# Kernel optimization log

Hardware: AMD Instinct MI355X
Metric: run time of the kernel (lower is better)

## Reference

```python
import jax, jax.numpy as jnp
import numpy as np

N_HEAD = 16

def setup_inputs() -> dict:
    key = jax.random.key(0)
    ks = jax.random.split(key, 5)
    B, S, D = 4, 2048, 1024
    return {
        "string": jax.random.normal(ks[0], (B, S, D), dtype=jnp.float32),
        "string_len": jax.random.randint(ks[1], (B,), 1, S + 1),
        "Wqkv": jax.random.normal(ks[2], (D, 3 * D), dtype=jnp.float32) * 0.02,
        "bqkv": jnp.zeros((3 * D,), dtype=jnp.float32),
        "Wo": jax.random.normal(ks[3], (D, D), dtype=jnp.float32) * 0.02,
        "bo": jnp.zeros((D,), dtype=jnp.float32),
    }


def reference(string, string_len, Wqkv, bqkv, Wo, bo):
    B, S, D = string.shape
    H = N_HEAD
    hd = D // H
    x = string @ Wqkv + bqkv                      # [B,S,3D]
    q, k, v = jnp.split(x, 3, axis=-1)
    # split heads -> [B,H,S,hd]
    q = q.reshape(B, S, H, hd).transpose(0, 2, 1, 3)
    k = k.reshape(B, S, H, hd).transpose(0, 2, 1, 3)
    v = v.reshape(B, S, H, hd).transpose(0, 2, 1, 3)
    w = jnp.einsum('bhqd,bhkd->bhqk', q, k) / jnp.sqrt(jnp.float32(hd))
    causal = jnp.tril(jnp.ones((S, S), dtype=bool))  # [S,S]
    w = jnp.where(causal[None, None], w, jnp.float32(-1e9))
    w = jax.nn.softmax(w, axis=-1)
    a = jnp.einsum('bhqk,bhkd->bhqd', w, v)       # [B,H,S,hd]
    a = a.transpose(0, 2, 1, 3).reshape(B, S, D)  # merge heads
    a = a @ Wo + bo
    return a, string_len
```

## Files before the change

### kernel.cpp

```cpp
#include <hip/hip_runtime.h>
#include <hip/hip_fp8.h>
#include <stdint.h>

typedef __attribute__((ext_vector_type(8))) short bf16x8;
typedef __attribute__((ext_vector_type(4))) float f32x4;
typedef __attribute__((ext_vector_type(16))) float f32x16;
typedef __attribute__((ext_vector_type(4))) unsigned short u16x4;

static constexpr int Bn = 4, Sn = 2048, Dn = 1024, Hn = 16, HD = 64;
static constexpr int Mrows = Bn * Sn;
static constexpr int D3 = 3 * Dn;

__device__ __forceinline__ unsigned short f2bf(float f) {
  unsigned int u = __float_as_uint(f);
  u += 0x7FFF + ((u >> 16) & 1);
  return (unsigned short)(u >> 16);
}

__device__ __forceinline__ unsigned char f2fp8(float f) {
  __hip_fp8_e4m3 v(f);
  return (unsigned char)v.__x;
}

__device__ __forceinline__ void gload16(const void* gptr, void* lptr) {
  __builtin_amdgcn_global_load_lds(
      (__attribute__((address_space(1))) void*)gptr,
      (__attribute__((address_space(3))) void*)lptr, 16, 0, 0);
}

__device__ __forceinline__ int swz8(int r) { return (r ^ (r >> 3)) & 7; }

__device__ __forceinline__ float vexp2(float x) {
#if __has_builtin(__builtin_amdgcn_exp2f)
  return __builtin_amdgcn_exp2f(x);
#else
  return exp2f(x);
#endif
}

__device__ __forceinline__ unsigned cvtpk(float lo, float hi) {
  unsigned r;
  asm("v_cvt_pk_bf16_f32 %0, %1, %2" : "=v"(r) : "v"(lo), "v"(hi));
  return r;
}

__device__ __forceinline__ float lanepull(float v, int srclane) {
  return __int_as_float(__builtin_amdgcn_ds_bpermute(srclane * 4, __float_as_int(v)));
}

__global__ void cvt_f32_fp8(const float* __restrict__ in,
                            unsigned char* __restrict__ out, int n) {
  int i = (blockIdx.x * blockDim.x + threadIdx.x) * 4;
  if (i < n) {
    const float4 v = *(const float4*)(in + i);
    uchar4 o;
    o.x = f2fp8(v.x); o.y = f2fp8(v.y); o.z = f2fp8(v.z); o.w = f2fp8(v.w);
    *(uchar4*)(out + i) = o;
  }
}

__global__ void transpose_cvt_fp8(const float* __restrict__ W,
                                  unsigned char* __restrict__ Wt, int K, int N) {
  __shared__ float tile[32][33];
  const int n0 = blockIdx.x * 32, k0 = blockIdx.y * 32;
  const int tx = threadIdx.x, ty = threadIdx.y;
  #pragma unroll
  for (int j = 0; j < 4; j++)
    tile[ty + 8 * j][tx] = W[(size_t)(k0 + ty + 8 * j) * N + n0 + tx];
  __syncthreads();
  #pragma unroll
  for (int j = 0; j < 4; j++)
    Wt[(size_t)(n0 + ty + 8 * j) * K + k0 + tx] = f2fp8(tile[tx][ty + 8 * j] * 64.0f);
}

template<bool BF16_OUT>
__global__ __launch_bounds__(512, 1)
void gemm_fp8(const unsigned char* __restrict__ A,
              const unsigned char* __restrict__ Bt,
              const float* __restrict__ bias,
              void* __restrict__ Cout, int Nt, int Kt) {
  __shared__ __align__(128) unsigned char smem[98304];
  const int tid = threadIdx.x;
  const int w = tid >> 6, lane = tid & 63;
  const int wm = w >> 2, wn = w & 3;
  const int lrow = lane & 15, lk = lane >> 4;
  const long brow = (long)blockIdx.x * 128;
  const long bcol = (long)blockIdx.y * 256;

  const int srow = tid >> 3;
  const int sslot = tid & 7;

  auto stage = [&](int k0, unsigned char* buf) {
    unsigned char* Ab = buf;
    unsigned char* Bb = buf + 16384;
    #pragma unroll
    for (int i = 0; i < 2; i++) {
      const int r = srow + 64 * i;
      gload16(A + (size_t)(brow + r) * Kt + k0 + ((sslot ^ swz8(r)) * 16),
              Ab + w * 1024 + i * 8192);
    }
    #pragma unroll
    for (int i = 0; i < 4; i++) {
      const int r = srow + 64 * i;
      gload16(Bt + (size_t)(bcol + r) * Kt + k0 + ((sslot ^ swz8(r)) * 16),
              Bb + w * 1024 + i * 8192);
    }
  };

  f32x4 acc[4][4] = {};

  stage(0, smem);

  const int ntile = Kt >> 7;
  for (int t = 0; t < ntile; t++) {
    const int cur = t & 1;
    unsigned char* Ab = smem + cur * 49152;
    unsigned char* Bb = Ab + 16384;

    __builtin_amdgcn_s_barrier();
    if (t + 1 < ntile) {
      stage((t + 1) << 7, smem + (cur ^ 1) * 49152);
      asm volatile("s_waitcnt vmcnt(6)");
    } else {
      asm volatile("s_waitcnt vmcnt(0)");
    }
    __builtin_amdgcn_sched_barrier(0);
    __builtin_amdgcn_s_barrier();

    const int sub = (lk & 1) * 8;
    #pragma unroll
    for (int kk = 0; kk < 4; kk++) {
      const int s16 = kk * 2 + (lk >> 1);
      long av[4], bv[4];
      #pragma unroll
      for (int mt = 0; mt < 4; mt++) {
        const int r = wm * 64 + mt * 16 + lrow;
        av[mt] = *(const long*)(Ab + r * 128 + (((s16 ^ swz8(r)) << 4) + sub));
      }
      #pragma unroll
      for (int nt = 0; nt < 4; nt++) {
        const int r = wn * 64 + nt * 16 + lrow;
        bv[nt] = *(const long*)(Bb + r * 128 + (((s16 ^ swz8(r)) << 4) + sub));
      }
      __builtin_amdgcn_s_setprio(1);
      #pragma unroll
      for (int mt = 0; mt < 4; mt++)
        #pragma unroll
        for (int nt = 0; nt < 4; nt++)
          acc[mt][nt] = __builtin_amdgcn_mfma_f32_16x16x32_fp8_fp8(av[mt], bv[nt], acc[mt][nt], 0, 0, 0);
      __builtin_amdgcn_s_setprio(0);
    }
  }

  #pragma unroll
  for (int nt = 0; nt < 4; nt++) {
    const long col = bcol + wn * 64 + nt * 16 + lrow;
    const float bv2 = bias[col];
    #pragma unroll
    for (int mt = 0; mt < 4; mt++) {
      #pragma unroll
      for (int rr = 0; rr < 4; rr++) {
        const long row = brow + wm * 64 + mt * 16 + lk * 4 + rr;
        const float v = acc[mt][nt][rr] * 0.015625f + bv2;
        if (BF16_OUT)
          ((unsigned short*)Cout)[row * Nt + col] = f2bf(v);
        else
          ((float*)Cout)[row * Nt + col] = v;
      }
    }
  }
}

__global__ __launch_bounds__(256, 2)
void attn_lpt(const unsigned short* __restrict__ QKV,
              unsigned char* __restrict__ Out) {
  __shared__ __align__(128) unsigned char smem[32768];
  const int tid  = threadIdx.x;
  const int w    = tid >> 6;
  const int lane = tid & 63;
  const int li = lane & 31, hi = lane >> 5;
  const int bh = blockIdx.x;
  const int b  = bh >> 4, h = bh & 15;
  const int m  = 15 - (int)blockIdx.y;
  const int wq = m * 128 + w * 32;
  const int qrow = wq + li;

  const float cexp = 0.18033688011112042f;

  bf16x8 qf[4];
  {
    const unsigned short* qp = QKV + (size_t)(b * Sn + qrow) * D3 + h * HD + hi * 8;
    #pragma unroll
    for (int ks = 0; ks < 4; ks++) qf[ks] = *(const bf16x8*)(qp + ks * 16);
  }

  f32x16 o0 = {}, o1 = {};
  float mm = -3.0e38f, ls = 0.f;

  unsigned char* Kb = smem;
  unsigned char* Vb = smem + 16384;

  auto kstage = [&](int kb) {
    #pragma unroll
    for (int i = 0; i < 4; i++) {
      const int r    = i * 32 + w * 8 + (lane >> 3);
      const int slot = (lane & 7) ^ swz8(r);
      gload16(QKV + (size_t)(b * Sn + kb + r) * D3 + Dn + h * HD + slot * 8,
              Kb + i * 4096 + w * 1024);
    }
  };
  const int vkv = tid >> 1;
  const int vd0 = (tid & 1) * 32;
  auto vload = [&](int kb, int jj) -> bf16x8 {
    return *(const bf16x8*)(QKV + (size_t)(b * Sn + kb + vkv) * D3 + 2 * Dn + h * HD + vd0 + jj * 8);
  };
  auto vwrite = [&](bf16x8 vv, int jj) {
    #pragma unroll
    for (int e = 0; e < 8; e++) {
      const int d  = vd0 + jj * 8 + e;
      const int vs = (d ^ (d >> 3)) & 15;
      *(unsigned short*)(Vb + d * 256 + (((vkv >> 3) ^ vs) << 4) + (vkv & 7) * 2) = (unsigned short)vv[e];
    }
  };

  auto substep = [&](int s, int kb) {
    f32x16 s0 = {}, s1 = {};
    const int r0 = s * 64 + li, r1 = s * 64 + 32 + li;
    __builtin_amdgcn_s_setprio(1);
    #pragma unroll
    for (int ks = 0; ks < 4; ks++) {
      const int slot = ks * 2 + hi;
      const bf16x8 k0 = *(const bf16x8*)(Kb + r0 * 128 + ((slot ^ swz8(r0)) * 16));
      const bf16x8 k1 = *(const bf16x8*)(Kb + r1 * 128 + ((slot ^ swz8(r1)) * 16));
      s0 = __builtin_amdgcn_mfma_f32_32x32x16_bf16(k0, qf[ks], s0, 0, 0, 0);
      s1 = __builtin_amdgcn_mfma_f32_32x32x16_bf16(k1, qf[ks], s1, 0, 0, 0);
    }
    __builtin_amdgcn_s_setprio(0);
    const int kbase = kb + s * 64;
    if (kbase + 63 > wq) {
      #pragma unroll
      for (int r = 0; r < 16; r++) {
        const int kvl = (r & 3) + 8 * (r >> 2) + 4 * hi;
        if (kbase + kvl > qrow)      s0[r] = -3.0e38f;
        if (kbase + 32 + kvl > qrow) s1[r] = -3.0e38f;
      }
    }
    float t8[8];
    #pragma unroll
    for (int r = 0; r < 8; r++)
      t8[r] = fmaxf(fmaxf(s0[r], s0[r + 8]), fmaxf(s1[r], s1[r + 8]));
    float tmax = fmaxf(fmaxf(fmaxf(t8[0], t8[1]), fmaxf(t8[2], t8[3])),
                       fmaxf(fmaxf(t8[4], t8[5]), fmaxf(t8[6], t8[7])));
    tmax = fmaxf(tmax, __shfl_xor(tmax, 32));
    if (__any(tmax > mm + 44.0f)) {
      const float mn   = fmaxf(mm, tmax);
      const float corr = vexp2((mm - mn) * cexp);
      mm = mn;
      ls *= corr;
      #pragma unroll
      for (int r = 0; r < 16; r++) {
        const float cr = lanepull(corr, (r & 3) + 8 * (r >> 2) + 4 * hi);
        o0[r] *= cr; o1[r] *= cr;
      }
    }
    const float mc = mm * cexp;
    f32x16 p0, p1;
    float psa = 0.f, psb = 0.f, psc = 0.f, psd = 0.f;
    #pragma unroll
    for (int r = 0; r < 16; r += 4) {
      p0[r] = vexp2(fmaf(s0[r], cexp, -mc));         psa += p0[r];
      p0[r + 1] = vexp2(fmaf(s0[r + 1], cexp, -mc)); psb += p0[r + 1];
      p0[r + 2] = vexp2(fmaf(s0[r + 2], cexp, -mc)); psc += p0[r + 2];
      p0[r + 3] = vexp2(fmaf(s0[r + 3], cexp, -mc)); psd += p0[r + 3];
    }
    #pragma unroll
    for (int r = 0; r < 16; r += 4) {
      p1[r] = vexp2(fmaf(s1[r], cexp, -mc));         psa += p1[r];
      p1[r + 1] = vexp2(fmaf(s1[r + 1], cexp, -mc)); psb += p1[r + 1];
      p1[r + 2] = vexp2(fmaf(s1[r + 2], cexp, -mc)); psc += p1[r + 2];
      p1[r + 3] = vexp2(fmaf(s1[r + 3], cexp, -mc)); psd += p1[r + 3];
    }
    ls += (psa + psb) + (psc + psd);

    auto mk_pa = [&](const f32x16& pp, int base) -> bf16x8 {
      const unsigned a0 = cvtpk(pp[base + 0], pp[base + 1]);
      const unsigned a1 = cvtpk(pp[base + 2], pp[base + 3]);
      const unsigned b0 = cvtpk(pp[base + 4], pp[base + 5]);
      const unsigned b1 = cvtpk(pp[base + 6], pp[base + 7]);
      const unsigned xa0 = __shfl_xor(a0, 32), xa1 = __shfl_xor(a1, 32);
      const unsigned xb0 = __shfl_xor(b0, 32), xb1 = __shfl_xor(b1, 32);
      union { unsigned u[4]; bf16x8 v; } pu;
      pu.u[0] = hi ? xb0 : a0;
      pu.u[1] = hi ? xb1 : a1;
      pu.u[2] = hi ? b0  : xa0;
      pu.u[3] = hi ? b1  : xa1;
      return pu.v;
    };
    bf16x8 pa[4];
    pa[0] = mk_pa(p0, 0); pa[1] = mk_pa(p0, 8);
    pa[2] = mk_pa(p1, 0); pa[3] = mk_pa(p1, 8);

    const int vs0 = (li ^ (li >> 3)) & 15;
    const int vs1 = ((32 + li) ^ ((32 + li) >> 3)) & 15;
    __builtin_amdgcn_s_setprio(1);
    #pragma unroll
    for (int k16 = 0; k16 < 4; k16++) {
      const int slot = s * 8 + k16 * 2 + hi;
      const bf16x8 vb0 = *(const bf16x8*)(Vb + li * 256 + ((slot ^ vs0) << 4));
      const bf16x8 vb1 = *(const bf16x8*)(Vb + (32 + li) * 256 + ((slot ^ vs1) << 4));
      o0 = __builtin_amdgcn_mfma_f32_32x32x16_bf16(pa[k16], vb0, o0, 0, 0, 0);
      o1 = __builtin_amdgcn_mfma_f32_32x32x16_bf16(pa[k16], vb1, o1, 0, 0, 0);
    }
    __builtin_amdgcn_s_setprio(0);
  };

  for (int t = 0; t <= m; t++) {
    const int kb = t << 7;
    __builtin_amdgcn_s_barrier();
    kstage(kb);
    {
      bf16x8 v0 = vload(kb, 0), v1 = vload(kb, 1), v2 = vload(kb, 2), v3 = vload(kb, 3);
      vwrite(v0, 0); vwrite(v1, 1); vwrite(v2, 2); vwrite(v3, 3);
    }
    asm volatile("s_waitcnt vmcnt(0) lgkmcnt(0)");
    __builtin_amdgcn_sched_barrier(0);
    __builtin_amdgcn_s_barrier();

    substep(0, kb);
    if (kb + 64 <= wq + 31) substep(1, kb);
  }

  const float lt = ls + __shfl_xor(ls, 32);
  const float rl = __builtin_amdgcn_rcpf(lt);
  #pragma unroll
  for (int r = 0; r < 16; r++) {
    const int q = (r & 3) + 8 * (r >> 2) + 4 * hi;
    const float rr = lanepull(rl, q);
    unsigned char* op = Out + (size_t)(b * Sn + wq + q) * Dn + h * HD;
    op[li]      = f2fp8(o0[r] * rr);
    op[32 + li] = f2fp8(o1[r] * rr);
  }
}

__global__ void copy_len(const int* __restrict__ slen, float* __restrict__ dst, int n) {
  const int i = threadIdx.x;
  if (i < n) dst[i] = (float)slen[i];
}

extern "C" void kernel_launch(void* const* d_in, const int* in_sizes, int n_in,
                              void* d_out, int out_size, void* d_ws, size_t ws_size,
                              hipStream_t stream) {
  const float* X    = (const float*)d_in[0];
  const int*   slen = (const int*)d_in[1];
  const float* Wqkv = (const float*)d_in[2];
  const float* bqkv = (const float*)d_in[3];
  const float* Wo   = (const float*)d_in[4];
  const float* bo   = (const float*)d_in[5];
  float* out = (float*)d_out;

  char* ws = (char*)d_ws;
  unsigned char*  Xf8   = (unsigned char*)ws;
  unsigned char*  Wtq8  = (unsigned char*)(ws + 16777216);
  unsigned char*  Wto8  = (unsigned char*)(ws + 16777216 + 6291456);
  unsigned short* QKVb  = (unsigned short*)(ws + 16777216 + 6291456 + 2097152);
  unsigned char*  Attnb = (unsigned char*)ws;

  cvt_f32_fp8<<<dim3(8192), dim3(256), 0, stream>>>(X, Xf8, Mrows * Dn);
  transpose_cvt_fp8<<<dim3(96, 32), dim3(32, 8), 0, stream>>>(Wqkv, Wtq8, Dn, D3);
  transpose_cvt_fp8<<<dim3(32, 32), dim3(32, 8), 0, stream>>>(Wo, Wto8, Dn, Dn);

  gemm_fp8<true><<<dim3(64, 12), dim3(512), 0, stream>>>(Xf8, Wtq8, bqkv, (void*)QKVb, D3, Dn);
  attn_lpt<<<dim3(64, 16), dim3(256), 0, stream>>>(QKVb, Attnb);
  gemm_fp8<false><<<dim3(64, 4), dim3(512), 0, stream>>>(Attnb, Wto8, bo, d_out, Dn, Dn);
  copy_len<<<dim3(1), dim3(64), 0, stream>>>(slen, out + (size_t)Mrows * Dn, Bn);
}
```

Measured before the change: 154.8 us.

## Double-buffer 64-row K/V tiles in attention to overlap loads with compute

The attention kernel's KV tile shrinks from 128 to 64 rows, and the 32KB LDS becomes two ping-pong buffers. The next tile's K (async global-to-LDS) and V (register loads) are issued before the current tile's MFMA work, and V is written to LDS afterwards. This hides global-load latency behind compute and leaves one barrier per iteration instead of two. V also gets a simpler 128-byte-row XOR swizzle. The trade-off is twice as many loop iterations. The kernel now relies on implicit vmcnt waits from the V register use to cover the async K loads.

```diff
diff --git a/kernel.cpp b/kernel.cpp
--- a/kernel.cpp
+++ b/kernel.cpp
@@ -172,8 +172,8 @@
 }
 
 __global__ __launch_bounds__(256, 2)
-void attn_lpt(const unsigned short* __restrict__ QKV,
-              unsigned char* __restrict__ Out) {
+void attn_lpt2(const unsigned short* __restrict__ QKV,
+               unsigned char* __restrict__ Out) {
   __shared__ __align__(128) unsigned char smem[32768];
   const int tid  = threadIdx.x;
   const int w    = tid >> 6;
@@ -197,35 +197,31 @@
   f32x16 o0 = {}, o1 = {};
   float mm = -3.0e38f, ls = 0.f;
 
-  unsigned char* Kb = smem;
-  unsigned char* Vb = smem + 16384;
-
-  auto kstage = [&](int kb) {
-    #pragma unroll
-    for (int i = 0; i < 4; i++) {
+  auto kstage = [&](int kb, unsigned char* Kb) {
+    #pragma unroll
+    for (int i = 0; i < 2; i++) {
       const int r    = i * 32 + w * 8 + (lane >> 3);
       const int slot = (lane & 7) ^ swz8(r);
       gload16(QKV + (size_t)(b * Sn + kb + r) * D3 + Dn + h * HD + slot * 8,
               Kb + i * 4096 + w * 1024);
     }
   };
-  const int vkv = tid >> 1;
-  const int vd0 = (tid & 1) * 32;
+  const int vkv = tid >> 2;
+  const int vd0 = (tid & 3) * 16;
   auto vload = [&](int kb, int jj) -> bf16x8 {
     return *(const bf16x8*)(QKV + (size_t)(b * Sn + kb + vkv) * D3 + 2 * Dn + h * HD + vd0 + jj * 8);
   };
-  auto vwrite = [&](bf16x8 vv, int jj) {
+  auto vwrite = [&](bf16x8 vv, int jj, unsigned char* Vb) {
     #pragma unroll
     for (int e = 0; e < 8; e++) {
-      const int d  = vd0 + jj * 8 + e;
-      const int vs = (d ^ (d >> 3)) & 15;
-      *(unsigned short*)(Vb + d * 256 + (((vkv >> 3) ^ vs) << 4) + (vkv & 7) * 2) = (unsigned short)vv[e];
-    }
-  };
-
-  auto substep = [&](int s, int kb) {
+      const int d = vd0 + jj * 8 + e;
+      *(unsigned short*)(Vb + d * 128 + ((vkv * 2) ^ (swz8(d) << 4))) = (unsigned short)vv[e];
+    }
+  };
+
+  auto substep = [&](int kb, const unsigned char* Kb, const unsigned char* Vb) {
     f32x16 s0 = {}, s1 = {};
-    const int r0 = s * 64 + li, r1 = s * 64 + 32 + li;
+    const int r0 = li, r1 = 32 + li;
     __builtin_amdgcn_s_setprio(1);
     #pragma unroll
     for (int ks = 0; ks < 4; ks++) {
@@ -236,13 +232,12 @@
       s1 = __builtin_amdgcn_mfma_f32_32x32x16_bf16(k1, qf[ks], s1, 0, 0, 0);
     }
     __builtin_amdgcn_s_setprio(0);
-    const int kbase = kb + s * 64;
-    if (kbase + 63 > wq) {
+    if (kb + 63 > wq) {
       #pragma unroll
       for (int r = 0; r < 16; r++) {
         const int kvl = (r & 3) + 8 * (r >> 2) + 4 * hi;
-        if (kbase + kvl > qrow)      s0[r] = -3.0e38f;
-        if (kbase + 32 + kvl > qrow) s1[r] = -3.0e38f;
+        if (kb + kvl > qrow)      s0[r] = -3.0e38f;
+        if (kb + 32 + kvl > qrow) s1[r] = -3.0e38f;
       }
     }
     float t8[8];
@@ -300,34 +295,52 @@
     pa[0] = mk_pa(p0, 0); pa[1] = mk_pa(p0, 8);
     pa[2] = mk_pa(p1, 0); pa[3] = mk_pa(p1, 8);
 
-    const int vs0 = (li ^ (li >> 3)) & 15;
-    const int vs1 = ((32 + li) ^ ((32 + li) >> 3)) & 15;
     __builtin_amdgcn_s_setprio(1);
     #pragma unroll
     for (int k16 = 0; k16 < 4; k16++) {
-      const int slot = s * 8 + k16 * 2 + hi;
-      const bf16x8 vb0 = *(const bf16x8*)(Vb + li * 256 + ((slot ^ vs0) << 4));
-      const bf16x8 vb1 = *(const bf16x8*)(Vb + (32 + li) * 256 + ((slot ^ vs1) << 4));
+      const int slot = k16 * 2 + hi;
+      const bf16x8 vb0 = *(const bf16x8*)(Vb + li * 128 + ((slot ^ swz8(li)) * 16));
+      const bf16x8 vb1 = *(const bf16x8*)(Vb + (32 + li) * 128 + ((slot ^ swz8(32 + li)) * 16));
       o0 = __builtin_amdgcn_mfma_f32_32x32x16_bf16(pa[k16], vb0, o0, 0, 0, 0);
       o1 = __builtin_amdgcn_mfma_f32_32x32x16_bf16(pa[k16], vb1, o1, 0, 0, 0);
     }
     __builtin_amdgcn_s_setprio(0);
   };
 
-  for (int t = 0; t <= m; t++) {
-    const int kb = t << 7;
+  kstage(0, smem);
+  {
+    bf16x8 v0 = vload(0, 0), v1 = vload(0, 1);
+    vwrite(v0, 0, smem + 8192);
+    vwrite(v1, 1, smem + 8192);
+  }
+  asm volatile("s_waitcnt lgkmcnt(0)");
+  __builtin_amdgcn_sched_barrier(0);
+
+  const int nt = 2 * m + 2;
+  for (int t = 0; t < nt; t++) {
+    const int kb  = t << 6;
+    const int cur = t & 1;
+    unsigned char* Kb = smem + cur * 16384;
+    unsigned char* Vb = Kb + 8192;
+    const bool pre = (t + 1 < nt);
+    bf16x8 vna, vnb;
+
     __builtin_amdgcn_s_barrier();
-    kstage(kb);
-    {
-      bf16x8 v0 = vload(kb, 0), v1 = vload(kb, 1), v2 = vload(kb, 2), v3 = vload(kb, 3);
-      vwrite(v0, 0); vwrite(v1, 1); vwrite(v2, 2); vwrite(v3, 3);
-    }
-    asm volatile("s_waitcnt vmcnt(0) lgkmcnt(0)");
+    if (pre) {
+      kstage(kb + 64, smem + (cur ^ 1) * 16384);
+      vna = vload(kb + 64, 0);
+      vnb = vload(kb + 64, 1);
+    }
+
+    if (kb <= wq + 31) substep(kb, Kb, Vb);
+
+    if (pre) {
+      unsigned char* Vn = smem + (cur ^ 1) * 16384 + 8192;
+      vwrite(vna, 0, Vn);
+      vwrite(vnb, 1, Vn);
+    }
+    asm volatile("s_waitcnt lgkmcnt(0)");
     __builtin_amdgcn_sched_barrier(0);
-    __builtin_amdgcn_s_barrier();
-
-    substep(0, kb);
-    if (kb + 64 <= wq + 31) substep(1, kb);
   }
 
   const float lt = ls + __shfl_xor(ls, 32);
@@ -370,7 +383,7 @@
   transpose_cvt_fp8<<<dim3(32, 32), dim3(32, 8), 0, stream>>>(Wo, Wto8, Dn, Dn);
 
   gemm_fp8<true><<<dim3(64, 12), dim3(512), 0, stream>>>(Xf8, Wtq8, bqkv, (void*)QKVb, D3, Dn);
-  attn_lpt<<<dim3(64, 16), dim3(256), 0, stream>>>(QKVb, Attnb);
+  attn_lpt2<<<dim3(64, 16), dim3(256), 0, stream>>>(QKVb, Attnb);
   gemm_fp8<false><<<dim3(64, 4), dim3(512), 0, stream>>>(Attnb, Wto8, bo, d_out, Dn, Dn);
   copy_len<<<dim3(1), dim3(64), 0, stream>>>(slen, out + (size_t)Mrows * Dn, Bn);
 }
```

After: 157.6 us. Within noise of the previous version (+1.8%).
